# Performance work log

Hardware: AMD Instinct MI355X
Metric: run time of the kernel (lower is better)

The kernel has to match this reference:

```python
import jax, jax.numpy as jnp
import numpy as np

EPS = 1e-05
MOMENTUM = 0.1


def inv_sqrtm(A, eps=1e-09):
    # torch.svd: A = U diag(S) V^T ; jnp.linalg.svd: A = U diag(S) Vh, so Vh == V^T
    U, S, Vh = jnp.linalg.svd(A)
    S = jnp.maximum(S, eps)
    return (U * (S ** -0.5)[None, :]) @ Vh


def setup_inputs() -> dict:
    key = jax.random.key(0)
    N, d = 262144, 512
    x = jax.random.normal(key, (N, d), dtype=jnp.float32)
    running_covar = jnp.eye(d, dtype=jnp.float32)
    return {"x": x, "running_covar": running_covar}


def reference(x, running_covar):
    # training-mode BatchWhiten with track_running_stats=True, momentum=0.1
    N = x.shape[0]
    covar = (x.T @ x) / N                       # [d, d]
    eaf = MOMENTUM
    running = running_covar * eaf + covar * (1.0 - eaf)
    covar = jnp.maximum(running, EPS)           # elementwise max, as in torch.max(covar, eps)
    B = inv_sqrtm(covar, EPS)                   # [d, d] inverse sqrt via SVD
    return x @ B                                # whitened input [N, d]
```

## Files before the change

kernel.cpp:

```cpp
#include <hip/hip_runtime.h>
#include <stdint.h>


#define N_ROWS 262144
#define D 512
#define NS_ITERS 3
#define CK_CHUNKS 128
#define CK_ROWS (N_ROWS / CK_CHUNKS)
#define BKC 32
#define CK_STEPS (CK_ROWS / BKC)

typedef float f32x4 __attribute__((ext_vector_type(4)));
typedef short s16x8 __attribute__((ext_vector_type(8)));
typedef short s16x4 __attribute__((ext_vector_type(4)));
typedef __bf16 bf16x8 __attribute__((ext_vector_type(8)));

static __device__ __forceinline__ unsigned short f2bf(float f) {
  unsigned u = __float_as_uint(f);
  u += 0x7FFFu + ((u >> 16) & 1u);
  return (unsigned short)(u >> 16);
}

static __device__ __forceinline__ f32x4 mfma16(s16x8 a, s16x8 b, f32x4 c) {
  return __builtin_amdgcn_mfma_f32_16x16x32_bf16(
      __builtin_bit_cast(bf16x8, a), __builtin_bit_cast(bf16x8, b), c, 0, 0, 0);
}

static __device__ __forceinline__ void gld_lds16(const void* g, void* l) {
  __builtin_amdgcn_global_load_lds(
      (const __attribute__((address_space(1))) void*)g,
      (__attribute__((address_space(3))) void*)l, 16, 0, 0);
}

#define SWZ4(c) (((c) ^ ((c) >> 2)) & 3)
#define SWZ8(c) (((c) ^ ((c) >> 3)) & 7)

static __device__ __forceinline__ void bar_lgkm() {
  asm volatile("s_waitcnt lgkmcnt(0)" ::: "memory");
  __builtin_amdgcn_s_barrier();
  __builtin_amdgcn_sched_barrier(0);
}

__global__ __launch_bounds__(256) void covar_k(const float* __restrict__ x,
                                               float* __restrict__ Cpart,
                                               short* __restrict__ xb16) {
  __shared__ short ldsA[2][128 * 32];
  __shared__ short ldsB[2][128 * 32];

  const int hw = blockIdx.x;
  const int work = (hw & 7) * 160 + (hw >> 3);
  int t = work % 10, mb = 0, rl = 4;
  while (t >= rl) { t -= rl; ++mb; --rl; }
  const int nb = mb + t;
  const int chunk = work / 10;
  float* C = Cpart + (size_t)(hw & 7) * (D * D);

  const int tid = threadIdx.x;
  const int c2 = (tid & 63) * 2;
  const int kh = tid >> 6;

  const int lane = tid & 63;
  const int wave = tid >> 6;
  const int wr = wave >> 1, wc = wave & 1;
  const int l15 = lane & 15, g = lane >> 4;

  const bool offd = (nb != mb);
  const bool haveDump = (xb16 != nullptr);
  const int rankA = nb - mb;
  const int rankB = 4 - (nb - mb);
  const bool dumpA = haveDump && (kh == rankA);
  const bool dumpB = haveDump && offd && (kh == rankB);
  uint32_t* xw = (uint32_t*)xb16;

  f32x4 acc[4][4];
#pragma unroll
  for (int i = 0; i < 4; ++i)
#pragma unroll
    for (int j = 0; j < 4; ++j) acc[i][j] = f32x4{0.f, 0.f, 0.f, 0.f};

  const size_t kbase0 = (size_t)chunk * CK_ROWS;

  float2 bufM[8], bufN[8];
  {
    const float* srcM = x + (kbase0 + kh * 8) * D + mb * 128 + c2;
#pragma unroll
    for (int q = 0; q < 8; ++q) bufM[q] = *(const float2*)(srcM + (size_t)q * D);
    if (offd) {
      const float* srcN = x + (kbase0 + kh * 8) * D + nb * 128 + c2;
#pragma unroll
      for (int q = 0; q < 8; ++q) bufN[q] = *(const float2*)(srcN + (size_t)q * D);
    }
  }

  for (int st = 0; st < CK_STEPS; ++st) {
    const size_t k0 = kbase0 + (size_t)st * BKC;

    s16x8 pM0, pM1, pN0, pN1;
#pragma unroll
    for (int q = 0; q < 8; ++q) {
      pM0[q] = (short)f2bf(bufM[q].x);
      pM1[q] = (short)f2bf(bufM[q].y);
    }
    if (offd) {
#pragma unroll
      for (int q = 0; q < 8; ++q) {
        pN0[q] = (short)f2bf(bufN[q].x);
        pN1[q] = (short)f2bf(bufN[q].y);
      }
    }

    if (st + 1 < CK_STEPS) {
      const float* srcM = x + (k0 + BKC + kh * 8) * D + mb * 128 + c2;
#pragma unroll
      for (int q = 0; q < 8; ++q)
        bufM[q] = *(const float2*)(srcM + (size_t)q * D);
      if (offd) {
        const float* srcN = x + (k0 + BKC + kh * 8) * D + nb * 128 + c2;
#pragma unroll
        for (int q = 0; q < 8; ++q)
          bufN[q] = *(const float2*)(srcN + (size_t)q * D);
      }
    }

    short* wA = ldsA[st & 1];
    short* wB = ldsB[st & 1];
    *(s16x8*)(wA + c2 * 32 + ((kh ^ SWZ4(c2)) << 3)) = pM0;
    *(s16x8*)(wA + (c2 + 1) * 32 + ((kh ^ SWZ4(c2 + 1)) << 3)) = pM1;
    if (offd) {
      *(s16x8*)(wB + c2 * 32 + ((kh ^ SWZ4(c2)) << 3)) = pN0;
      *(s16x8*)(wB + (c2 + 1) * 32 + ((kh ^ SWZ4(c2 + 1)) << 3)) = pN1;
    }
    if (dumpA) {
#pragma unroll
      for (int q = 0; q < 8; ++q) {
        const uint32_t u =
            (uint32_t)(uint16_t)pM0[q] | ((uint32_t)(uint16_t)pM1[q] << 16);
        __builtin_nontemporal_store(
            u, &xw[(k0 + kh * 8 + q) * 256 + mb * 64 + (c2 >> 1)]);
      }
    }
    if (dumpB) {
#pragma unroll
      for (int q = 0; q < 8; ++q) {
        const uint32_t u =
            (uint32_t)(uint16_t)pN0[q] | ((uint32_t)(uint16_t)pN1[q] << 16);
        __builtin_nontemporal_store(
            u, &xw[(k0 + kh * 8 + q) * 256 + nb * 64 + (c2 >> 1)]);
      }
    }

    bar_lgkm();

    const short* rA = ldsA[st & 1];
    const short* rB = offd ? ldsB[st & 1] : ldsA[st & 1];
    s16x8 af[4], bfv[4];
#pragma unroll
    for (int mi = 0; mi < 4; ++mi) {
      const int m = 64 * wr + 16 * mi + l15;
      af[mi] = *(const s16x8*)(rA + m * 32 + ((g ^ SWZ4(m)) << 3));
    }
#pragma unroll
    for (int nj = 0; nj < 4; ++nj) {
      const int n = 64 * wc + 16 * nj + l15;
      bfv[nj] = *(const s16x8*)(rB + n * 32 + ((g ^ SWZ4(n)) << 3));
    }
#pragma unroll
    for (int mi = 0; mi < 4; ++mi)
#pragma unroll
      for (int nj = 0; nj < 4; ++nj)
        acc[mi][nj] = mfma16(af[mi], bfv[nj], acc[mi][nj]);
  }

#pragma unroll
  for (int mi = 0; mi < 4; ++mi)
#pragma unroll
    for (int nj = 0; nj < 4; ++nj) {
      const int n = nb * 128 + 64 * wc + 16 * nj + l15;
#pragma unroll
      for (int r = 0; r < 4; ++r) {
        const int m = mb * 128 + 64 * wr + 16 * mi + 4 * g + r;
        atomicAdd(&C[(size_t)m * D + n], acc[mi][nj][r]);
      }
    }
}

__global__ __launch_bounds__(256) void prep_k(const float* __restrict__ Cpart,
                                              const float* __restrict__ run,
                                              float* __restrict__ M,
                                              unsigned* __restrict__ sMax) {
  const int r = blockIdx.x;
  const int t = threadIdx.x;
  const float cs = 0.9f / (float)N_ROWS;
  float sum = 0.f;
  for (int c = t; c < D; c += 256) {
    const int rr = r < c ? r : c;
    const int cc = r < c ? c : r;
    float cv = 0.f;
#pragma unroll
    for (int p = 0; p < 8; ++p)
      cv += Cpart[(size_t)p * D * D + (size_t)rr * D + cc];
    float v = 0.1f * run[(size_t)r * D + c] + cs * cv;
    v = fmaxf(v, 1e-5f);
    M[(size_t)r * D + c] = v;
    sum += v;
  }
  __shared__ float red[256];
  red[t] = sum;
  __syncthreads();
  for (int off = 128; off > 0; off >>= 1) {
    if (t < off) red[t] += red[t + off];
    __syncthreads();
  }
  if (t == 0) atomicMax(sMax, __float_as_uint(red[0]));
}

__global__ __launch_bounds__(256) void init2_k(const float* __restrict__ M,
                                               const unsigned* __restrict__ sMax,
                                               float* __restrict__ Y0,
                                               float* __restrict__ T,
                                               float* __restrict__ Z1) {
  const float inv = 1.0f / __uint_as_float(*sMax);
  const int i0 = (blockIdx.x * 256 + threadIdx.x) * 4;
  const float4 m4 = *(const float4*)&M[i0];
  const int row = i0 >> 9, col0 = i0 & 511;
  float y[4], tv[4];
#pragma unroll
  for (int e = 0; e < 4; ++e) {
    y[e] = (&m4.x)[e] * inv;
    tv[e] = (row == col0 + e ? 1.5f : 0.f) - 0.5f * y[e];
  }
  *(float4*)&Y0[i0] = make_float4(y[0], y[1], y[2], y[3]);
  const float4 t4 = make_float4(tv[0], tv[1], tv[2], tv[3]);
  *(float4*)&T[i0] = t4;
  *(float4*)&Z1[i0] = t4;
}

__device__ __forceinline__ void mm512_body(const float* __restrict__ A,
                                           const float* __restrict__ B,
                                           float* a00, float* a01, float* a10,
                                           float* a11, int rbase, int cbase) {
  __shared__ float As[32][36];
  __shared__ float Bs[32][36];
  const int t = threadIdx.x;
  const int tx = t & 15, ty = t >> 4;
  const int sr = t >> 3, sc = (t & 7) * 4;
  float c00 = 0.f, c01 = 0.f, c10 = 0.f, c11 = 0.f;
  for (int k0 = 0; k0 < D; k0 += 32) {
    __syncthreads();
    *(float4*)&As[sr][sc] = *(const float4*)(A + (size_t)(rbase + sr) * D + k0 + sc);
    *(float4*)&Bs[sr][sc] = *(const float4*)(B + (size_t)(k0 + sr) * D + cbase + sc);
    __syncthreads();
#pragma unroll
    for (int kk = 0; kk < 32; ++kk) {
      const float av0 = As[2 * ty][kk], av1 = As[2 * ty + 1][kk];
      const float2 bv = *(const float2*)&Bs[kk][2 * tx];
      c00 = fmaf(av0, bv.x, c00);
      c01 = fmaf(av0, bv.y, c01);
      c10 = fmaf(av1, bv.x, c10);
      c11 = fmaf(av1, bv.y, c11);
    }
  }
  *a00 = c00; *a01 = c01; *a10 = c10; *a11 = c11;
}

__global__ __launch_bounds__(256) void mmY_k(const float* __restrict__ A,
                                             const float* __restrict__ B,
                                             float* __restrict__ O) {
  const int rbase = blockIdx.y * 32, cbase = blockIdx.x * 32;
  float a00, a01, a10, a11;
  mm512_body(A, B, &a00, &a01, &a10, &a11, rbase, cbase);
  const int tx = threadIdx.x & 15, ty = threadIdx.x >> 4;
  const int r0 = rbase + 2 * ty, c0 = cbase + 2 * tx;
  O[(size_t)r0 * D + c0] = a00;
  O[(size_t)r0 * D + c0 + 1] = a01;
  O[(size_t)(r0 + 1) * D + c0] = a10;
  O[(size_t)(r0 + 1) * D + c0 + 1] = a11;
}

__global__ __launch_bounds__(256) void mmT_k(const float* __restrict__ Zm,
                                             const float* __restrict__ Ym,
                                             float* __restrict__ T) {
  const int rbase = blockIdx.y * 32, cbase = blockIdx.x * 32;
  float a00, a01, a10, a11;
  mm512_body(Zm, Ym, &a00, &a01, &a10, &a11, rbase, cbase);
  const int tx = threadIdx.x & 15, ty = threadIdx.x >> 4;
  const int r0 = rbase + 2 * ty, c0 = cbase + 2 * tx;
  T[(size_t)r0 * D + c0] = (r0 == c0 ? 1.5f : 0.f) - 0.5f * a00;
  T[(size_t)r0 * D + c0 + 1] = (r0 == c0 + 1 ? 1.5f : 0.f) - 0.5f * a01;
  T[(size_t)(r0 + 1) * D + c0] = (r0 + 1 == c0 ? 1.5f : 0.f) - 0.5f * a10;
  T[(size_t)(r0 + 1) * D + c0 + 1] = (r0 + 1 == c0 + 1 ? 1.5f : 0.f) - 0.5f * a11;
}

__global__ __launch_bounds__(256) void mmpair_k(const float* __restrict__ Y,
                                                const float* __restrict__ Z,
                                                const float* __restrict__ T,
                                                float* __restrict__ Yn,
                                                float* __restrict__ Zn) {
  const float* A = blockIdx.z ? T : Y;
  const float* B = blockIdx.z ? Z : T;
  float* O = blockIdx.z ? Zn : Yn;
  const int rbase = blockIdx.y * 32, cbase = blockIdx.x * 32;
  float a00, a01, a10, a11;
  mm512_body(A, B, &a00, &a01, &a10, &a11, rbase, cbase);
  const int tx = threadIdx.x & 15, ty = threadIdx.x >> 4;
  const int r0 = rbase + 2 * ty, c0 = cbase + 2 * tx;
  O[(size_t)r0 * D + c0] = a00;
  O[(size_t)r0 * D + c0 + 1] = a01;
  O[(size_t)(r0 + 1) * D + c0] = a10;
  O[(size_t)(r0 + 1) * D + c0 + 1] = a11;
}

__global__ __launch_bounds__(256) void mmZp_k(const float* __restrict__ T,
                                              const float* __restrict__ Z,
                                              const unsigned* __restrict__ sMax,
                                              short* __restrict__ panels) {
  const int rbase = blockIdx.y * 32, cbase = blockIdx.x * 32;
  float a00, a01, a10, a11;
  mm512_body(T, Z, &a00, &a01, &a10, &a11, rbase, cbase);
  const float rs = rsqrtf(__uint_as_float(*sMax));
  const int tx = threadIdx.x & 15, ty = threadIdx.x >> 4;
  const int r0 = rbase + 2 * ty, c0 = cbase + 2 * tx;
  const float vv[2][2] = {{a00, a01}, {a10, a11}};
#pragma unroll
  for (int dr = 0; dr < 2; ++dr)
#pragma unroll
    for (int dc = 0; dc < 2; ++dc) {
      const int k = r0 + dr, n = c0 + dc;
      const int nb_ = n >> 7, nl = n & 127;
      const int ks = k >> 6, kl = k & 63;
      const int ch = (kl >> 3) ^ SWZ8(nl), e = kl & 7;
      const size_t pi = (size_t)((nb_ * 8 + ks) * 128 + nl) * 64 + ch * 8 + e;
      panels[pi] = (short)f2bf(vv[dr][dc] * rs);
    }
}

__global__ __launch_bounds__(256) void gemm_k(const short* __restrict__ xb16,
                                              const short* __restrict__ panels,
                                              float* __restrict__ out) {
  __shared__ short lds[4][128 * 64];

  const int hw = blockIdx.x;
  const int q = hw & 7, j = hw >> 3;
  const int ct = j & 3;
  const int rp = ((j >> 2) << 3) | q;
  const size_t rbase = (size_t)rp * 128;

  const int tid = threadIdx.x;
  const int lane = tid & 63, wave = tid >> 6;
  const int wr = wave >> 1, wc = wave & 1;
  const int l15 = lane & 15, g = lane >> 4;
  const int wrow0 = 32 * wave;

  f32x4 acc[4][4];
#pragma unroll
  for (int i = 0; i < 4; ++i)
#pragma unroll
    for (int j2 = 0; j2 < 4; ++j2) acc[i][j2] = f32x4{0.f, 0.f, 0.f, 0.f};

  auto STAGE = [&](int buf, int ksv) {
#pragma unroll
    for (int i = 0; i < 4; ++i) {
      const int m = wrow0 + 8 * i + (lane >> 3);
      const short* src = xb16 + (rbase + m) * D + ksv * 64 +
                         (((lane & 7) ^ SWZ8(m)) << 3);
      gld_lds16(src, &lds[buf][(wrow0 + 8 * i) * 64]);
    }
    const short* srcB = panels + ((size_t)(ct * 8 + ksv) << 13);
#pragma unroll
    for (int i = 0; i < 4; ++i)
      gld_lds16(srcB + wave * 2048 + i * 512 + lane * 8,
                &lds[2 + buf][wave * 2048 + i * 512]);
  };

  STAGE(0, 0);

  for (int ks = 0; ks < 8; ++ks) {
    const int cur = ks & 1;
    if (ks < 7) {
      STAGE(cur ^ 1, ks + 1);
      asm volatile("s_waitcnt vmcnt(8)" ::: "memory");
    } else {
      asm volatile("s_waitcnt vmcnt(0)" ::: "memory");
    }
    __builtin_amdgcn_s_barrier();
    __builtin_amdgcn_sched_barrier(0);

    const short* rA = lds[cur];
    const short* rB = lds[2 + cur];
#pragma unroll
    for (int kk = 0; kk < 2; ++kk) {
      s16x8 af[4], bfv[4];
#pragma unroll
      for (int mi = 0; mi < 4; ++mi) {
        const int m = 64 * wr + 16 * mi + l15;
        af[mi] = *(const s16x8*)(rA + m * 64 + ((((kk << 2) | g) ^ SWZ8(m)) << 3));
      }
#pragma unroll
      for (int nj = 0; nj < 4; ++nj) {
        const int n = 64 * wc + 16 * nj + l15;
        bfv[nj] = *(const s16x8*)(rB + n * 64 + ((((kk << 2) | g) ^ SWZ8(n)) << 3));
      }
#pragma unroll
      for (int mi = 0; mi < 4; ++mi)
#pragma unroll
        for (int nj = 0; nj < 4; ++nj)
          acc[mi][nj] = mfma16(af[mi], bfv[nj], acc[mi][nj]);
    }

    asm volatile("s_waitcnt lgkmcnt(0)" ::: "memory");
    __builtin_amdgcn_s_barrier();
    __builtin_amdgcn_sched_barrier(0);
  }

  float* scratch = (float*)&lds[0][0];
  const int wbase = wave * 1088;
#pragma unroll
  for (int mi = 0; mi < 4; ++mi) {
#pragma unroll
    for (int nj = 0; nj < 4; ++nj)
#pragma unroll
      for (int r = 0; r < 4; ++r)
        scratch[wbase + (4 * g + r) * 68 + 16 * nj + l15] = acc[mi][nj][r];
    __syncthreads();
#pragma unroll
    for (int i = 0; i < 4; ++i) {
      const int rl = g + 4 * i;
      const f32x4 v = *(const f32x4*)&scratch[wbase + rl * 68 + l15 * 4];
      const size_t row_g = rbase + 64 * wr + 16 * mi + rl;
      const int col_g = ct * 128 + 64 * wc + l15 * 4;
      __builtin_nontemporal_store(v, (f32x4*)(out + row_g * D + col_g));
    }
    __syncthreads();
  }
}

__global__ __launch_bounds__(256) void gemm_fb_k(const float* __restrict__ x,
                                                 const short* __restrict__ panels,
                                                 float* __restrict__ out) {
  __shared__ short lds[2 * 128 * 64];
  short* ldsA = lds;
  short* ldsB = lds + 128 * 64;

  const int hw = blockIdx.x;
  const int q = hw & 7, j = hw >> 3;
  const int ct = j & 3;
  const int rp = ((j >> 2) << 3) | q;
  const size_t rbase = (size_t)rp * 128;

  const int tid = threadIdx.x;
  const int lane = tid & 63, wave = tid >> 6;
  const int wr = wave >> 1, wc = wave & 1;
  const int l15 = lane & 15, g = lane >> 4;

  const int mb8 = tid >> 4;
  const int koff = (tid & 15) * 4;
  const int chA = koff >> 3, subA = koff & 7;

  f32x4 acc[4][4];
#pragma unroll
  for (int i = 0; i < 4; ++i)
#pragma unroll
    for (int j2 = 0; j2 < 4; ++j2) acc[i][j2] = f32x4{0.f, 0.f, 0.f, 0.f};

  for (int ks = 0; ks < 8; ++ks) {
    __syncthreads();
#pragma unroll
    for (int i = 0; i < 8; ++i) {
      const int m = mb8 + (i << 4);
      const float4 v = *(const float4*)(x + (rbase + m) * D + ks * 64 + koff);
      s16x4 p;
      p[0] = (short)f2bf(v.x);
      p[1] = (short)f2bf(v.y);
      p[2] = (short)f2bf(v.z);
      p[3] = (short)f2bf(v.w);
      *(s16x4*)(ldsA + m * 64 + ((chA ^ SWZ8(m)) << 3) + subA) = p;
    }
    {
      const short* src = panels + ((size_t)(ct * 8 + ks) << 13);
#pragma unroll
      for (int i = 0; i < 4; ++i)
        gld_lds16(src + wave * 2048 + i * 512 + lane * 8,
                  ldsB + wave * 2048 + i * 512);
    }
    __syncthreads();

#pragma unroll
    for (int kk = 0; kk < 2; ++kk) {
      s16x8 af[4], bfv[4];
#pragma unroll
      for (int mi = 0; mi < 4; ++mi) {
        const int m = 64 * wr + 16 * mi + l15;
        af[mi] = *(const s16x8*)(ldsA + m * 64 + ((((kk << 2) | g) ^ SWZ8(m)) << 3));
      }
#pragma unroll
      for (int nj = 0; nj < 4; ++nj) {
        const int n = 64 * wc + 16 * nj + l15;
        bfv[nj] = *(const s16x8*)(ldsB + n * 64 + ((((kk << 2) | g) ^ SWZ8(n)) << 3));
      }
#pragma unroll
      for (int mi = 0; mi < 4; ++mi)
#pragma unroll
        for (int nj = 0; nj < 4; ++nj)
          acc[mi][nj] = mfma16(af[mi], bfv[nj], acc[mi][nj]);
    }
  }

  __syncthreads();
  float* scratch = (float*)lds;
  const int wbase = wave * 1088;
#pragma unroll
  for (int mi = 0; mi < 4; ++mi) {
#pragma unroll
    for (int nj = 0; nj < 4; ++nj)
#pragma unroll
      for (int r = 0; r < 4; ++r)
        scratch[wbase + (4 * g + r) * 68 + 16 * nj + l15] = acc[mi][nj][r];
    __syncthreads();
#pragma unroll
    for (int i = 0; i < 4; ++i) {
      const int rl = g + 4 * i;
      const f32x4 v = *(const f32x4*)&scratch[wbase + rl * 68 + l15 * 4];
      const size_t row_g = rbase + 64 * wr + 16 * mi + rl;
      const int col_g = ct * 128 + 64 * wc + l15 * 4;
      __builtin_nontemporal_store(v, (f32x4*)(out + row_g * D + col_g));
    }
    __syncthreads();
  }
}

extern "C" void kernel_launch(void* const* d_in, const int* in_sizes, int n_in,
                              void* d_out, int out_size, void* d_ws,
                              size_t ws_size, hipStream_t stream) {
  (void)in_sizes; (void)n_in; (void)out_size;
  const float* x = (const float*)d_in[0];
  const float* run = (const float*)d_in[1];
  float* out = (float*)d_out;
  uint8_t* ws = (uint8_t*)d_ws;

  float* Cpart = (float*)ws;
  unsigned* sMax = (unsigned*)(ws + (8u << 20));
  float* M = (float*)(ws + (8u << 20) + 256);
  float* Ya = M + 262144;
  float* Yb = Ya + 262144;
  float* Za = Yb + 262144;
  float* Zb = Za + 262144;
  float* T = Zb + 262144;
  short* panels = (short*)(T + 262144);
  short* xb16 = panels + 262144;

  const size_t need =
      (size_t)((uint8_t*)xb16 - ws) + (size_t)N_ROWS * D * sizeof(short);
  const bool big = ws_size >= need;

  (void)hipMemsetAsync(Cpart, 0, (8u << 20) + 256, stream);

  covar_k<<<1280, 256, 0, stream>>>(x, Cpart, big ? xb16 : nullptr);
  prep_k<<<512, 256, 0, stream>>>(Cpart, run, M, sMax);

  init2_k<<<256, 256, 0, stream>>>(M, sMax, Ya, T, Za);
  mmY_k<<<dim3(16, 16), 256, 0, stream>>>(Ya, T, Yb);

  float *Y = Yb, *Z = Za, *Yn = Ya, *Zn = Zb;
  for (int it = 1; it < NS_ITERS - 1; ++it) {
    mmT_k<<<dim3(16, 16), 256, 0, stream>>>(Z, Y, T);
    mmpair_k<<<dim3(16, 16, 2), 256, 0, stream>>>(Y, Z, T, Yn, Zn);
    float* t1 = Y; Y = Yn; Yn = t1;
    t1 = Z; Z = Zn; Zn = t1;
  }

  mmT_k<<<dim3(16, 16), 256, 0, stream>>>(Z, Y, T);
  mmZp_k<<<dim3(16, 16), 256, 0, stream>>>(T, Z, sMax, panels);

  if (big)
    gemm_k<<<8192, 256, 0, stream>>>(xb16, panels, out);
  else
    gemm_fb_k<<<8192, 256, 0, stream>>>(x, panels, out);
}
```

Baseline: 610.6 us.

## Split covariance staging across 512 threads with per-tile waves and new LDS swizzle

The covariance kernel goes from 256 to 512 threads per block. Half the waves stage the M column tile and half stage the N tile, so each thread converts and stores one tile instead of two. Each wave now computes a 64x32 output sub-tile rather than 64x64, which halves accumulator registers and raises parallelism per block. The LDS layout uses a new 8-way XOR swizzle to match the new access pattern. On diagonal blocks the B-staging waves sit idle during staging, and more waves share each barrier.

```diff
diff --git a/kernel.cpp b/kernel.cpp
--- a/kernel.cpp
+++ b/kernel.cpp
@@ -32,8 +32,10 @@
       (__attribute__((address_space(3))) void*)l, 16, 0, 0);
 }
 
-#define SWZ4(c) (((c) ^ ((c) >> 2)) & 3)
 #define SWZ8(c) (((c) ^ ((c) >> 3)) & 7)
+
+#define CVOFF(c, kc) \
+  ((((c) >> 1) << 6) + ((((((kc) << 1) | ((c) & 1))) ^ SWZ8((c) >> 1)) << 3))
 
 static __device__ __forceinline__ void bar_lgkm() {
   asm volatile("s_waitcnt lgkmcnt(0)" ::: "memory");
@@ -41,11 +43,10 @@
   __builtin_amdgcn_sched_barrier(0);
 }
 
-__global__ __launch_bounds__(256) void covar_k(const float* __restrict__ x,
+__global__ __launch_bounds__(512) void covar_k(const float* __restrict__ x,
                                                float* __restrict__ Cpart,
                                                short* __restrict__ xb16) {
-  __shared__ short ldsA[2][128 * 32];
-  __shared__ short ldsB[2][128 * 32];
+  __shared__ short ldsT[2][2][128 * 32];
 
   const int hw = blockIdx.x;
   const int work = (hw & 7) * 160 + (hw >> 3);
@@ -56,126 +57,94 @@
   float* C = Cpart + (size_t)(hw & 7) * (D * D);
 
   const int tid = threadIdx.x;
-  const int c2 = (tid & 63) * 2;
-  const int kh = tid >> 6;
-
   const int lane = tid & 63;
   const int wave = tid >> 6;
-  const int wr = wave >> 1, wc = wave & 1;
+  const int isB = wave >> 2;
+  const int kh = wave & 3;
+  const int c2 = lane * 2;
+
+  const int wr = wave >> 2, wc = wave & 3;
   const int l15 = lane & 15, g = lane >> 4;
 
   const bool offd = (nb != mb);
+  const bool doStage = (!isB) || offd;
+  const int tileCol = (isB ? nb : mb) * 128;
+
   const bool haveDump = (xb16 != nullptr);
-  const int rankA = nb - mb;
-  const int rankB = 4 - (nb - mb);
-  const bool dumpA = haveDump && (kh == rankA);
-  const bool dumpB = haveDump && offd && (kh == rankB);
+  const int rank = isB ? (4 - (nb - mb)) : (nb - mb);
+  const bool dump = haveDump && doStage && (kh == rank);
   uint32_t* xw = (uint32_t*)xb16;
 
-  f32x4 acc[4][4];
+  f32x4 acc[4][2];
 #pragma unroll
   for (int i = 0; i < 4; ++i)
 #pragma unroll
-    for (int j = 0; j < 4; ++j) acc[i][j] = f32x4{0.f, 0.f, 0.f, 0.f};
+    for (int j = 0; j < 2; ++j) acc[i][j] = f32x4{0.f, 0.f, 0.f, 0.f};
 
   const size_t kbase0 = (size_t)chunk * CK_ROWS;
-
-  float2 bufM[8], bufN[8];
-  {
-    const float* srcM = x + (kbase0 + kh * 8) * D + mb * 128 + c2;
-#pragma unroll
-    for (int q = 0; q < 8; ++q) bufM[q] = *(const float2*)(srcM + (size_t)q * D);
-    if (offd) {
-      const float* srcN = x + (kbase0 + kh * 8) * D + nb * 128 + c2;
-#pragma unroll
-      for (int q = 0; q < 8; ++q) bufN[q] = *(const float2*)(srcN + (size_t)q * D);
-    }
+  const float* srcBase = x + (kbase0 + kh * 8) * D + tileCol + c2;
+
+  float2 buf[8];
+  if (doStage) {
+#pragma unroll
+    for (int q = 0; q < 8; ++q) buf[q] = *(const float2*)(srcBase + (size_t)q * D);
   }
 
   for (int st = 0; st < CK_STEPS; ++st) {
-    const size_t k0 = kbase0 + (size_t)st * BKC;
-
-    s16x8 pM0, pM1, pN0, pN1;
-#pragma unroll
-    for (int q = 0; q < 8; ++q) {
-      pM0[q] = (short)f2bf(bufM[q].x);
-      pM1[q] = (short)f2bf(bufM[q].y);
-    }
-    if (offd) {
+    if (doStage) {
+      s16x8 p0, p1;
 #pragma unroll
       for (int q = 0; q < 8; ++q) {
-        pN0[q] = (short)f2bf(bufN[q].x);
-        pN1[q] = (short)f2bf(bufN[q].y);
-      }
-    }
-
-    if (st + 1 < CK_STEPS) {
-      const float* srcM = x + (k0 + BKC + kh * 8) * D + mb * 128 + c2;
-#pragma unroll
-      for (int q = 0; q < 8; ++q)
-        bufM[q] = *(const float2*)(srcM + (size_t)q * D);
-      if (offd) {
-        const float* srcN = x + (k0 + BKC + kh * 8) * D + nb * 128 + c2;
-#pragma unroll
-        for (int q = 0; q < 8; ++q)
-          bufN[q] = *(const float2*)(srcN + (size_t)q * D);
-      }
-    }
-
-    short* wA = ldsA[st & 1];
-    short* wB = ldsB[st & 1];
-    *(s16x8*)(wA + c2 * 32 + ((kh ^ SWZ4(c2)) << 3)) = pM0;
-    *(s16x8*)(wA + (c2 + 1) * 32 + ((kh ^ SWZ4(c2 + 1)) << 3)) = pM1;
-    if (offd) {
-      *(s16x8*)(wB + c2 * 32 + ((kh ^ SWZ4(c2)) << 3)) = pN0;
-      *(s16x8*)(wB + (c2 + 1) * 32 + ((kh ^ SWZ4(c2 + 1)) << 3)) = pN1;
-    }
-    if (dumpA) {
-#pragma unroll
-      for (int q = 0; q < 8; ++q) {
-        const uint32_t u =
-            (uint32_t)(uint16_t)pM0[q] | ((uint32_t)(uint16_t)pM1[q] << 16);
-        __builtin_nontemporal_store(
-            u, &xw[(k0 + kh * 8 + q) * 256 + mb * 64 + (c2 >> 1)]);
-      }
-    }
-    if (dumpB) {
-#pragma unroll
-      for (int q = 0; q < 8; ++q) {
-        const uint32_t u =
-            (uint32_t)(uint16_t)pN0[q] | ((uint32_t)(uint16_t)pN1[q] << 16);
-        __builtin_nontemporal_store(
-            u, &xw[(k0 + kh * 8 + q) * 256 + nb * 64 + (c2 >> 1)]);
+        p0[q] = (short)f2bf(buf[q].x);
+        p1[q] = (short)f2bf(buf[q].y);
+      }
+      if (st + 1 < CK_STEPS) {
+        const float* src = srcBase + (size_t)(st + 1) * BKC * D;
+#pragma unroll
+        for (int q = 0; q < 8; ++q) buf[q] = *(const float2*)(src + (size_t)q * D);
+      }
+      short* wp = ldsT[st & 1][isB];
+      *(s16x8*)(wp + CVOFF(c2, kh)) = p0;
+      *(s16x8*)(wp + CVOFF(c2 + 1, kh)) = p1;
+      if (dump) {
+        const size_t k0 = kbase0 + (size_t)st * BKC;
+#pragma unroll
+        for (int q = 0; q < 8; ++q) {
+          const uint32_t u =
+              (uint32_t)(uint16_t)p0[q] | ((uint32_t)(uint16_t)p1[q] << 16);
+          __builtin_nontemporal_store(
+              u, &xw[(k0 + kh * 8 + q) * 256 + (tileCol >> 1) + lane]);
+        }
       }
     }
 
     bar_lgkm();
 
-    const short* rA = ldsA[st & 1];
-    const short* rB = offd ? ldsB[st & 1] : ldsA[st & 1];
-    s16x8 af[4], bfv[4];
+    const short* rA = ldsT[st & 1][0];
+    const short* rB = ldsT[st & 1][offd ? 1 : 0];
+    s16x8 af[4], bfv[2];
 #pragma unroll
     for (int mi = 0; mi < 4; ++mi) {
       const int m = 64 * wr + 16 * mi + l15;
-      af[mi] = *(const s16x8*)(rA + m * 32 + ((g ^ SWZ4(m)) << 3));
-    }
-#pragma unroll
-    for (int nj = 0; nj < 4; ++nj) {
-      const int n = 64 * wc + 16 * nj + l15;
-      bfv[nj] = *(const s16x8*)(rB + n * 32 + ((g ^ SWZ4(n)) << 3));
+      af[mi] = *(const s16x8*)(rA + CVOFF(m, g));
+    }
+#pragma unroll
+    for (int nj = 0; nj < 2; ++nj) {
+      const int n = 32 * wc + 16 * nj + l15;
+      bfv[nj] = *(const s16x8*)(rB + CVOFF(n, g));
     }
 #pragma unroll
     for (int mi = 0; mi < 4; ++mi)
 #pragma unroll
-      for (int nj = 0; nj < 4; ++nj)
+      for (int nj = 0; nj < 2; ++nj)
         acc[mi][nj] = mfma16(af[mi], bfv[nj], acc[mi][nj]);
   }
 
 #pragma unroll
   for (int mi = 0; mi < 4; ++mi)
 #pragma unroll
-    for (int nj = 0; nj < 4; ++nj) {
-      const int n = nb * 128 + 64 * wc + 16 * nj + l15;
+    for (int nj = 0; nj < 2; ++nj) {
+      const int n = nb * 128 + 32 * wc + 16 * nj + l15;
 #pragma unroll
       for (int r = 0; r < 4; ++r) {
         const int m = mb * 128 + 64 * wr + 16 * mi + 4 * g + r;
@@ -554,7 +523,7 @@
 
   (void)hipMemsetAsync(Cpart, 0, (8u << 20) + 256, stream);
 
-  covar_k<<<1280, 256, 0, stream>>>(x, Cpart, big ? xb16 : nullptr);
+  covar_k<<<1280, 512, 0, stream>>>(x, Cpart, big ? xb16 : nullptr);
   prep_k<<<512, 256, 0, stream>>>(Cpart, run, M, sMax);
 
   init2_k<<<256, 256, 0, stream>>>(M, sMax, Ya, T, Za);
```

Result: faster. 590.2 us (-3.3%).
